# Performance work log

Hardware: AMD Instinct MI355X
Metric: run time of the kernel (lower is better)

Reference implementation:

```python
import jax, jax.numpy as jnp
import numpy as np

B, C, H, W = 16, 64, 32, 32
E, HEADS, FF, L = 64, 4, 256, 3
NO_UNIT, INB = 6, 58
LN_EPS = 1e-5


def setup_inputs() -> dict:
    key = jax.random.key(0)
    ks = jax.random.split(key, 16)
    x = jax.random.normal(ks[0], (B, C, H, W), jnp.float32)
    # channel 58 = in-bounds everywhere; channel 6 = no-unit flag (Bernoulli 0.5)
    x = x.at[:, INB].set(1.0)
    x = x.at[:, NO_UNIT].set(jax.random.bernoulli(ks[1], 0.5, (B, H, W)).astype(jnp.float32))
    s = 0.05
    return {
        'x': x,
        'embed_w': jax.random.normal(ks[2], (C + 2, E), jnp.float32) * s,
        'embed_b': jnp.zeros((E,), jnp.float32),
        'ln1_w': jnp.ones((L, E), jnp.float32),
        'ln1_b': jnp.zeros((L, E), jnp.float32),
        'in_proj_w': jax.random.normal(ks[3], (L, 3 * E, E), jnp.float32) * s,
        'in_proj_b': jnp.zeros((L, 3 * E), jnp.float32),
        'out_w': jax.random.normal(ks[4], (L, E, E), jnp.float32) * s,
        'out_b': jnp.zeros((L, E), jnp.float32),
        'ln2_w': jnp.ones((L, E), jnp.float32),
        'ln2_b': jnp.zeros((L, E), jnp.float32),
        'ff1_w': jax.random.normal(ks[5], (L, E, FF), jnp.float32) * s,
        'ff1_b': jnp.zeros((L, FF), jnp.float32),
        'ff2_w': jax.random.normal(ks[6], (L, FF, E), jnp.float32) * s,
        'ff2_b': jnp.zeros((L, E), jnp.float32),
    }


def _layer_norm(x, w, b):
    mu = jnp.mean(x, axis=-1, keepdims=True)
    var = jnp.mean(jnp.square(x - mu), axis=-1, keepdims=True)
    return (x - mu) * jax.lax.rsqrt(var + LN_EPS) * w + b


def reference(x, embed_w, embed_b, ln1_w, ln1_b, in_proj_w, in_proj_b,
              out_w, out_b, ln2_w, ln2_b, ff1_w, ff1_b, ff2_w, ff2_b):
    Bn, Cn, Hn, Wn = x.shape
    S = Hn * Wn
    # position features (H == W here, matching torch tile/t() layout)
    ly = jnp.linspace(-1.0, 1.0, Hn)
    lx = jnp.linspace(-1.0, 1.0, Wn)
    pos = jnp.stack([jnp.tile(ly, (Wn, 1)), jnp.tile(lx, (Hn, 1)).T], axis=0)  # [2,H,W]
    xf = jnp.concatenate([x, jnp.broadcast_to(pos, (Bn, 2, Hn, Wn))], axis=1)
    xs = xf.reshape(Bn, Cn + 2, S).transpose(0, 2, 1)  # [B,S,C+2]

    # empty-space mask + vectorized squash (stable sort packs kept tokens first)
    empty = (xs[..., NO_UNIT] != 0) & (xs[..., INB] != 0)  # True = empty/masked
    keep = ~empty
    order = jnp.argsort(empty.astype(jnp.int32), axis=1, stable=True)  # [B,S]
    x_sq = jnp.take_along_axis(xs, order[:, :, None], axis=1)  # [B,S,C+2]
    n_keep = jnp.sum(keep, axis=1)
    pad = jnp.arange(S)[None, :] >= n_keep[:, None]  # True = padded key
    # (torch squashes to max(n_keep); padding to S is mathematically identical
    #  since padded rows are masked as keys and discarded on unsquash)
    bias = jnp.where(pad, -1e30, 0.0)[:, None, None, :]  # [B,1,1,S]

    h = x_sq @ embed_w + embed_b  # [B,S,E]
    dh = E // HEADS
    scale = 1.0 / float(np.sqrt(dh))
    for l in range(L):
        # identity_map_reordering: pre-norm attention
        a_in = _layer_norm(h, ln1_w[l], ln1_b[l])
        qkv = a_in @ in_proj_w[l].T + in_proj_b[l]
        q, k, v = jnp.split(qkv, 3, axis=-1)
        q = q.reshape(Bn, S, HEADS, dh)
        k = k.reshape(Bn, S, HEADS, dh)
        v = v.reshape(Bn, S, HEADS, dh)
        scores = jnp.einsum('bqhd,bkhd->bhqk', q, k) * scale + bias
        attn = jax.nn.softmax(scores, axis=-1)
        o = jnp.einsum('bhqk,bkhd->bqhd', attn, v).reshape(Bn, S, E)
        h = h + (o @ out_w[l].T + out_b[l])
        # pre-norm feed-forward (exact GELU, as nn.GELU default)
        f_in = _layer_norm(h, ln2_w[l], ln2_b[l])
        ff = jax.nn.gelu(f_in @ ff1_w[l] + ff1_b[l], approximate=False) @ ff2_w[l] + ff2_b[l]
        h = h + ff

    # unsquash: inverse permutation, zero at empty positions
    inv = jnp.argsort(order, axis=1)
    out = jnp.take_along_axis(h, inv[:, :, None], axis=1) * keep[:, :, None].astype(h.dtype)
    return out.transpose(0, 2, 1).reshape(Bn, E, Hn, Wn)
```

## Files before the change

kernel.cpp:

```cpp
#include <hip/hip_runtime.h>
#include <hip/hip_bf16.h>


#define BB 16
#define SS 1024
#define NT (BB*SS)

typedef short bf8 __attribute__((ext_vector_type(8)));
typedef float f4 __attribute__((ext_vector_type(4)));
typedef unsigned short u16;
typedef unsigned short us4 __attribute__((ext_vector_type(4)));

#define MFMA(a,b,c) __builtin_amdgcn_mfma_f32_16x16x32_bf16(a,b,c,0,0,0)

__device__ __forceinline__ float b2f(u16 u){
  union { unsigned int i; float f; } v; v.i = ((unsigned int)u) << 16; return v.f;
}
__device__ __forceinline__ u16 f2b(float f){
  union { float f; unsigned int i; } v; v.f = f;
  unsigned int x = v.i;
  return (u16)((x + 0x7FFFu + ((x >> 16) & 1u)) >> 16);
}
__device__ __forceinline__ unsigned int pkbf2(float a, float b){
  __hip_bfloat162 h = __float22bfloat162_rn(make_float2(a, b));
  union { __hip_bfloat162 h; unsigned int u; } c; c.h = h; return c.u;
}
__device__ __forceinline__ int probe_f32(const void* ln1w){
  return ((const u16*)ln1w)[0] == 0;
}
__device__ __forceinline__ float ldf(const void* p, int i, int isf32){
  return isf32 ? ((const float*)p)[i] : b2f(((const u16*)p)[i]);
}
__device__ __forceinline__ bf8 ldbf8(const void* p, int idx, int isf32){
  if (!isf32) return *(const bf8*)((const u16*)p + idx);
  const float4* s = (const float4*)((const float*)p + idx);
  float4 v0 = s[0], v1 = s[1];
  bf8 r;
  r[0] = (short)f2b(v0.x); r[1] = (short)f2b(v0.y);
  r[2] = (short)f2b(v0.z); r[3] = (short)f2b(v0.w);
  r[4] = (short)f2b(v1.x); r[5] = (short)f2b(v1.y);
  r[6] = (short)f2b(v1.z); r[7] = (short)f2b(v1.w);
  return r;
}
__device__ __forceinline__ float gelu(float x){
  float y = 1.5957691216f * x * (1.f + 0.044715f * x * x);
  float e = __expf(y);
  return x - x * __builtin_amdgcn_rcpf(e + 1.f);
}

#define O_L1W  64
#define O_L1B  256
#define O_IPW  448
#define O_IPB  37312
#define O_OW   37888
#define O_OWB  50176
#define O_L2W  50368
#define O_L2B  50560
#define O_F1B  50752
#define O_F2B  51520

__device__ __forceinline__ void cv(u16* dst, const void* src, int n, int isf32,
                                   int tid, int nth){
  if (isf32){
    const float* s = (const float*)src;
    for (int i = tid; i < n; i += nth) dst[i] = f2b(s[i]);
  } else {
    const u16* s = (const u16*)src;
    for (int i = tid; i < n; i += nth) dst[i] = s[i];
  }
}

__device__ __forceinline__ void qkv_core(bf8 a0, bf8 a1, bf8 b0, bf8 b1,
    int j, float bj, int lane, int bb4, int sw,
    u16* __restrict__ qb, u16* __restrict__ kb, u16* __restrict__ vt)
{
  int quad = lane >> 4;
  f4 acc = {0.f,0.f,0.f,0.f};
  acc = MFMA(a0, b0, acc);
  acc = MFMA(a1, b1, acc);
  if (j < 128){
    u16* dst = (j < 64) ? qb : kb;
    int jj = j & 63; int hd = jj >> 4, d = jj & 15;
    int base = (bb4 + hd)*1024 + sw + quad*4;
    #pragma unroll
    for (int r = 0; r < 4; r++) dst[((base + r) << 4) + d] = f2b(acc[r] + bj);
  } else {
    int jj = j - 128; int hd = jj >> 4, d = jj & 15;
    us4 pk;
    #pragma unroll
    for (int r = 0; r < 4; r++) pk[r] = f2b(acc[r] + bj);
    *(us4*)(vt + ((bb4 + hd)*16 + d)*1024 + sw + quad*4) = pk;
  }
}

__device__ __forceinline__ void ln_to_lds(const f4* hf, int lane,
    const u16* __restrict__ w, const u16* __restrict__ bs, u16* als)
{
  int col = lane & 15, quad = lane >> 4;
  float sm[4], sq[4];
  #pragma unroll
  for (int r = 0; r < 4; r++){
    float a = 0.f, q2 = 0.f;
    #pragma unroll
    for (int f = 0; f < 4; f++){ float v = hf[f][r]; a += v; q2 += v*v; }
    sm[r] = a; sq[r] = q2;
  }
  #pragma unroll
  for (int off = 1; off < 16; off <<= 1){
    #pragma unroll
    for (int r = 0; r < 4; r++){
      sm[r] += __shfl_xor(sm[r], off, 64);
      sq[r] += __shfl_xor(sq[r], off, 64);
    }
  }
  #pragma unroll
  for (int r = 0; r < 4; r++){
    float m = sm[r] * 0.015625f;
    float rstd = rsqrtf(fmaxf(sq[r]*0.015625f - m*m, 0.f) + 1e-5f);
    sm[r] = m; sq[r] = rstd;
  }
  #pragma unroll
  for (int f = 0; f < 4; f++){
    int n = f*16 + col;
    float ww = b2f(w[n]), bb = b2f(bs[n]);
    #pragma unroll
    for (int r = 0; r < 4; r++)
      als[(quad*4 + r)*72 + n] = f2b((hf[f][r] - sm[r])*sq[r]*ww + bb);
  }
}

__device__ __forceinline__ void ln4(f4 val, int wave, int col, int quad,
    const u16* __restrict__ w, const u16* __restrict__ bs,
    u16* als, float (*lnred)[16][2])
{
  float sm[4], sq[4];
  #pragma unroll
  for (int r = 0; r < 4; r++){ sm[r] = val[r]; sq[r] = val[r]*val[r]; }
  #pragma unroll
  for (int off = 1; off < 16; off <<= 1){
    #pragma unroll
    for (int r = 0; r < 4; r++){
      sm[r] += __shfl_xor(sm[r], off, 64);
      sq[r] += __shfl_xor(sq[r], off, 64);
    }
  }
  if (col == 0){
    #pragma unroll
    for (int r = 0; r < 4; r++){
      lnred[wave][quad*4 + r][0] = sm[r];
      lnred[wave][quad*4 + r][1] = sq[r];
    }
  }
  __syncthreads();
  int n = wave*16 + col;
  float ww = b2f(w[n]), bb = b2f(bs[n]);
  #pragma unroll
  for (int r = 0; r < 4; r++){
    int row = quad*4 + r;
    float s0 = lnred[0][row][0] + lnred[1][row][0] + lnred[2][row][0] + lnred[3][row][0];
    float q0 = lnred[0][row][1] + lnred[1][row][1] + lnred[2][row][1] + lnred[3][row][1];
    float m = s0 * 0.015625f;
    float rs = rsqrtf(fmaxf(q0*0.015625f - m*m, 0.f) + 1e-5f);
    als[row*72 + n] = f2b((val[r] - m)*rs*ww + bb);
  }
}

__global__ __launch_bounds__(256) void k0(
    const void* __restrict__ x,    const void* __restrict__ ewS,
    const void* __restrict__ ebS,  const void* __restrict__ l1wS,
    const void* __restrict__ l1bS, const void* __restrict__ ipwS,
    const void* __restrict__ ipbS, const void* __restrict__ owS,
    const void* __restrict__ owbS, const void* __restrict__ l2wS,
    const void* __restrict__ l2bS, const void* __restrict__ f1wS,
    const void* __restrict__ f1bS, const void* __restrict__ f2wS,
    const void* __restrict__ f2bS,
    u16* __restrict__ cb, u16* __restrict__ f1t, u16* __restrict__ f2t,
    float* __restrict__ h, int* __restrict__ nk, u16* __restrict__ cidx,
    u16* __restrict__ qb, u16* __restrict__ kb, u16* __restrict__ vt,
    void* __restrict__ outp, int out_elems)
{
  __shared__ __align__(16) u16 xs[4][16*104];
  __shared__ __align__(16) u16 als[4][16*72];
  __shared__ __align__(16) u16 ews[64*96];
  __shared__ __align__(16) u16 wsm[384];
  __shared__ int wtot[4];
  __shared__ u16 lcidx[1024];
  int tid = threadIdx.x;
  int lane = tid & 63, wave = tid >> 6;
  int col = lane & 15, quad = lane >> 4;
  int isf32 = probe_f32(l1wS);

  if (blockIdx.x >= 256){
    int gtid = (blockIdx.x - 256)*256 + tid;
    int nth  = 768*256;
    for (int i = gtid; i < 3*256*64; i += nth){
      int l = i / (256*64); int r = i % (256*64); int n = r / 64, k = r % 64;
      f1t[i] = f2b(ldf(f1wS, (l*64 + k)*256 + n, isf32));
    }
    for (int i = gtid; i < 3*64*256; i += nth){
      int l = i / (64*256); int r = i % (64*256); int n = r / 256, k = r % 256;
      f2t[i] = f2b(ldf(f2wS, (l*256 + k)*64 + n, isf32));
    }
    cv(cb + O_L1W, l1wS, 192,   isf32, gtid, nth);
    cv(cb + O_L1B, l1bS, 192,   isf32, gtid, nth);
    cv(cb + O_IPW, ipwS, 36864, isf32, gtid, nth);
    cv(cb + O_IPB, ipbS, 576,   isf32, gtid, nth);
    cv(cb + O_OW,  owS,  12288, isf32, gtid, nth);
    cv(cb + O_OWB, owbS, 192,   isf32, gtid, nth);
    cv(cb + O_L2W, l2wS, 192,   isf32, gtid, nth);
    cv(cb + O_L2B, l2bS, 192,   isf32, gtid, nth);
    cv(cb + O_F1B, f1bS, 768,   isf32, gtid, nth);
    cv(cb + O_F2B, f2bS, 192,   isf32, gtid, nth);
    int words = isf32 ? out_elems : (out_elems >> 1);
    unsigned int* op = (unsigned int*)outp;
    for (int i = gtid; i < words; i += nth) op[i] = 0u;
    return;
  }

  int b = blockIdx.x >> 4;
  int seg = blockIdx.x & 15;

  int kpl[4]; int c = 0;
  #pragma unroll
  for (int j = 0; j < 4; j++){
    int s4 = tid*4 + j;
    float x6  = ldf(x, ((b << 6) + 6)*1024 + s4, isf32);
    float x58 = ldf(x, ((b << 6) + 58)*1024 + s4, isf32);
    int k = (x6 != 0.f && x58 != 0.f) ? 0 : 1;
    kpl[j] = k; c += k;
  }
  #pragma unroll
  for (int j = 0; j < 4; j++) lcidx[tid*4 + j] = 0;
  int incl = c;
  #pragma unroll
  for (int off = 1; off < 64; off <<= 1){
    int v = __shfl_up(incl, off, 64);
    if (lane >= off) incl += v;
  }
  if (lane == 63) wtot[wave] = incl;
  __syncthreads();
  int prefix = 0;
  #pragma unroll
  for (int w2 = 0; w2 < 4; w2++) if (w2 < wave) prefix += wtot[w2];
  int excl = prefix + incl - c;
  int total = wtot[0] + wtot[1] + wtot[2] + wtot[3];
  {
    int p = excl;
    #pragma unroll
    for (int j = 0; j < 4; j++)
      if (kpl[j]){ lcidx[p] = (u16)(tid*4 + j); p++; }
  }
  __syncthreads();
  if (seg == 0){
    #pragma unroll
    for (int j = 0; j < 4; j++){
      int idx = tid*4 + j;
      cidx[(b << 10) + idx] = lcidx[idx];
    }
    if (tid == 0) nk[b] = total;
  }
  int base = seg * 64;
  if (base >= total) return;

  for (int i = tid; i < 64*96; i += 256){
    int n = i / 96, cc = i - n*96;
    ews[i] = (cc < 66) ? f2b(ldf(ewS, cc*64 + n, isf32)) : (u16)0;
  }
  for (int i = tid; i < 384; i += 256){
    float v;
    if (i < 64)       v = ldf(ebS,  i,       isf32);
    else if (i < 128) v = ldf(l1wS, i - 64,  isf32);
    else if (i < 192) v = ldf(l1bS, i - 128, isf32);
    else              v = ldf(ipbS, i - 192, isf32);
    wsm[i] = f2b(v);
  }
  __syncthreads();

  int slot0 = base + wave*16;
  int slotc = slot0 + col;
  int s = lcidx[slotc];
  u16* axs = xs[wave];
  #pragma unroll
  for (int i = 0; i < 16; i++){
    int cch = quad*16 + i;
    axs[col*104 + cch] = f2b(ldf(x, ((b << 6) + cch)*1024 + s, isf32));
  }
  #pragma unroll
  for (int i = 0; i < 8; i++){
    int cch = 64 + quad*8 + i;
    float v = 0.f;
    if (cch == 64)      v = -1.f + (2.f/31.f)*(float)(s & 31);
    else if (cch == 65) v = -1.f + (2.f/31.f)*(float)((s >> 5) & 31);
    axs[col*104 + cch] = f2b(v);
  }
  bf8 af[3];
  #pragma unroll
  for (int kc = 0; kc < 3; kc++) af[kc] = *(const bf8*)(axs + col*104 + kc*32 + quad*8);
  f4 hf[4];
  #pragma unroll
  for (int f = 0; f < 4; f++){
    f4 acc = {0.f,0.f,0.f,0.f};
    #pragma unroll
    for (int kc = 0; kc < 3; kc++){
      bf8 bfr = *(const bf8*)(ews + (f*16+col)*96 + kc*32 + quad*8);
      acc = MFMA(af[kc], bfr, acc);
    }
    float bias = b2f(wsm[f*16 + col]);
    #pragma unroll
    for (int r = 0; r < 4; r++){
      acc[r] += bias;
      h[((b << 10) + slot0 + quad*4 + r)*64 + f*16 + col] = acc[r];
    }
    hf[f] = acc;
  }
  ln_to_lds(hf, lane, wsm + 64, wsm + 128, als[wave]);
  bf8 a0 = *(const bf8*)(als[wave] + col*72 + quad*8);
  bf8 a1 = *(const bf8*)(als[wave] + col*72 + 32 + quad*8);
  #pragma unroll
  for (int jt = 0; jt < 12; jt++){
    int j = jt*16 + col;
    bf8 b0 = ldbf8(ipwS, (jt*16+col)*64 + quad*8, isf32);
    bf8 b1 = ldbf8(ipwS, (jt*16+col)*64 + 32 + quad*8, isf32);
    qkv_core(a0, a1, b0, b1, j, b2f(wsm[192 + j]), lane, b << 2, slot0, qb, kb, vt);
  }
}

__global__ __launch_bounds__(256) void k_layer(
    float* __restrict__ h, const u16* __restrict__ cb, int l, int nl,
    const u16* __restrict__ f1l, const u16* __restrict__ f2l,
    const u16* __restrict__ qbR, const u16* __restrict__ kbR,
    const u16* __restrict__ vtR,
    u16* __restrict__ qbW, u16* __restrict__ kbW, u16* __restrict__ vtW,
    const int* __restrict__ nk, const u16* __restrict__ cidx,
    void* __restrict__ outp, const void* __restrict__ dtype_probe, int last)
{
  __shared__ __align__(16) u16 smem[6528];
  __shared__ float lnred[4][16][2];
  u16* plds = smem;
  u16* gls  = smem;
  u16* ols  = smem + 4224;
  u16* als  = smem + 5376;

  int tid = threadIdx.x;
  int lane = tid & 63, wave = tid >> 6;
  int col = lane & 15, quad = lane >> 4;
  int b = blockIdx.x >> 6;
  int tb = (blockIdx.x & 63) * 16;
  int total = nk[b];
  if (tb >= total) return;
  int nfull = total & ~31;
  int tw = (b << 10) + tb;

  {
    int bh = (b << 2) + wave;
    const u16* qbase = qbR + (bh << 14);
    const u16* kbase = kbR + (bh << 14);
    const u16* vbase = vtR + (bh << 14);
    bf8 qf = {0,0,0,0,0,0,0,0};
    if (quad < 2) qf = *(const bf8*)(qbase + ((tb + col) << 4) + quad*8);
    f4 oacc = {0.f,0.f,0.f,0.f};
    float l4v[4] = {0.f,0.f,0.f,0.f};
    u16* pw = plds + wave*640;
    int kc = 0;
    for (; kc < nfull; kc += 32){
      bf8 vf = *(const bf8*)(vbase + col*1024 + kc + quad*8);
      #pragma unroll
      for (int t = 0; t < 2; t++){
        bf8 kf = {0,0,0,0,0,0,0,0};
        if (quad < 2) kf = *(const bf8*)(kbase + ((kc + t*16 + col) << 4) + quad*8);
        f4 sc = {0.f,0.f,0.f,0.f};
        sc = MFMA(qf, kf, sc);
        float p0 = __expf(fminf(sc[0]*0.25f, 60.f));
        float p1 = __expf(fminf(sc[1]*0.25f, 60.f));
        float p2 = __expf(fminf(sc[2]*0.25f, 60.f));
        float p3 = __expf(fminf(sc[3]*0.25f, 60.f));
        l4v[0] += p0; l4v[1] += p1; l4v[2] += p2; l4v[3] += p3;
        unsigned int u01 = pkbf2(p0, p1), u23 = pkbf2(p2, p3);
        int off = t*16 + col;
        pw[(quad*4 + 0)*40 + off] = (u16)u01;
        pw[(quad*4 + 1)*40 + off] = (u16)(u01 >> 16);
        pw[(quad*4 + 2)*40 + off] = (u16)u23;
        pw[(quad*4 + 3)*40 + off] = (u16)(u23 >> 16);
      }
      bf8 pf = *(const bf8*)(pw + col*40 + quad*8);
      oacc = MFMA(pf, vf, oacc);
    }
    if (kc < total){
      bf8 vf = *(const bf8*)(vbase + col*1024 + kc + quad*8);
      #pragma unroll
      for (int t = 0; t < 2; t++){
        bf8 kf = {0,0,0,0,0,0,0,0};
        int key = kc + t*16 + col;
        if (quad < 2) kf = *(const bf8*)(kbase + (key << 4) + quad*8);
        f4 sc = {0.f,0.f,0.f,0.f};
        sc = MFMA(qf, kf, sc);
        float kpv = (key < total) ? 1.f : 0.f;
        float p0 = kpv * __expf(fminf(sc[0]*0.25f, 60.f));
        float p1 = kpv * __expf(fminf(sc[1]*0.25f, 60.f));
        float p2 = kpv * __expf(fminf(sc[2]*0.25f, 60.f));
        float p3 = kpv * __expf(fminf(sc[3]*0.25f, 60.f));
        l4v[0] += p0; l4v[1] += p1; l4v[2] += p2; l4v[3] += p3;
        unsigned int u01 = pkbf2(p0, p1), u23 = pkbf2(p2, p3);
        int off = t*16 + col;
        pw[(quad*4 + 0)*40 + off] = (u16)u01;
        pw[(quad*4 + 1)*40 + off] = (u16)(u01 >> 16);
        pw[(quad*4 + 2)*40 + off] = (u16)u23;
        pw[(quad*4 + 3)*40 + off] = (u16)(u23 >> 16);
      }
      bf8 pf = *(const bf8*)(pw + col*40 + quad*8);
      oacc = MFMA(pf, vf, oacc);
    }
    #pragma unroll
    for (int off = 1; off < 16; off <<= 1)
      #pragma unroll
      for (int r = 0; r < 4; r++) l4v[r] += __shfl_xor(l4v[r], off, 64);
    #pragma unroll
    for (int r = 0; r < 4; r++){
      float rd = __builtin_amdgcn_rcpf(fmaxf(l4v[r], 1e-30f));
      ols[(quad*4 + r)*72 + wave*16 + col] = f2b(oacc[r] * rd);
    }
  }
  __syncthreads();

  {
    const u16* ow     = cb + O_OW  + l*4096;
    const u16* obias  = cb + O_OWB + l*64;
    const u16* f1b    = cb + O_F1B + l*256;
    const u16* f2bias = cb + O_F2B + l*64;
    int f = wave;
    bf8 af0 = *(const bf8*)(ols + col*72 + quad*8);
    bf8 af1 = *(const bf8*)(ols + col*72 + 32 + quad*8);
    f4 acc = {0.f,0.f,0.f,0.f};
    acc = MFMA(af0, *(const bf8*)(ow + (f*16+col)*64 + quad*8), acc);
    acc = MFMA(af1, *(const bf8*)(ow + (f*16+col)*64 + 32 + quad*8), acc);
    float bo = b2f(obias[f*16 + col]);
    f4 hfA;
    #pragma unroll
    for (int r = 0; r < 4; r++)
      hfA[r] = h[(tw + quad*4 + r)*64 + f*16 + col] + acc[r] + bo;
    ln4(hfA, wave, col, quad, cb + O_L2W + l*64, cb + O_L2B + l*64, als, lnred);
    __syncthreads();
    bf8 a0 = *(const bf8*)(als + col*72 + quad*8);
    bf8 a1 = *(const bf8*)(als + col*72 + 32 + quad*8);
    #pragma unroll
    for (int j = 0; j < 4; j++){
      int ft = wave*4 + j;
      f4 fa = {0.f,0.f,0.f,0.f};
      fa = MFMA(a0, *(const bf8*)(f1l + (ft*16+col)*64 + quad*8), fa);
      fa = MFMA(a1, *(const bf8*)(f1l + (ft*16+col)*64 + 32 + quad*8), fa);
      int n = ft*16 + col;
      float bb = b2f(f1b[n]);
      float g0 = gelu(fa[0] + bb), g1 = gelu(fa[1] + bb);
      float g2 = gelu(fa[2] + bb), g3 = gelu(fa[3] + bb);
      unsigned int u01 = pkbf2(g0, g1), u23 = pkbf2(g2, g3);
      gls[(quad*4 + 0)*264 + n] = (u16)u01;
      gls[(quad*4 + 1)*264 + n] = (u16)(u01 >> 16);
      gls[(quad*4 + 2)*264 + n] = (u16)u23;
      gls[(quad*4 + 3)*264 + n] = (u16)(u23 >> 16);
    }
    __syncthreads();
    bf8 gfr[8];
    #pragma unroll
    for (int kc = 0; kc < 8; kc++)
      gfr[kc] = *(const bf8*)(gls + col*264 + kc*32 + quad*8);
    f4 acc2 = {0.f,0.f,0.f,0.f};
    #pragma unroll
    for (int kc = 0; kc < 8; kc++)
      acc2 = MFMA(gfr[kc], *(const bf8*)(f2l + (f*16+col)*256 + kc*32 + quad*8), acc2);
    float b2v = b2f(f2bias[f*16 + col]);
    f4 hv;
    #pragma unroll
    for (int r = 0; r < 4; r++)
      hv[r] = hfA[r] + acc2[r] + b2v;
    if (last){
      int isf32 = probe_f32(dtype_probe);
      #pragma unroll
      for (int r = 0; r < 4; r++){
        int slot = tb + quad*4 + r;
        if (slot < total){
          int s = cidx[(b << 10) + slot];
          long idx = (long)((b << 6) + f*16 + col)*1024 + s;
          if (isf32) ((float*)outp)[idx] = hv[r];
          else       ((u16*)outp)[idx]   = f2b(hv[r]);
        }
      }
    } else {
      #pragma unroll
      for (int r = 0; r < 4; r++)
        h[(tw + quad*4 + r)*64 + f*16 + col] = hv[r];
      ln4(hv, wave, col, quad, cb + O_L1W + nl*64, cb + O_L1B + nl*64, als, lnred);
      __syncthreads();
      const u16* ipw = cb + O_IPW + nl*12288;
      const u16* ipb = cb + O_IPB + nl*192;
      bf8 qa0 = *(const bf8*)(als + col*72 + quad*8);
      bf8 qa1 = *(const bf8*)(als + col*72 + 32 + quad*8);
      #pragma unroll
      for (int j = 0; j < 3; j++){
        int jt = wave*3 + j;
        int jj = jt*16 + col;
        bf8 b0 = *(const bf8*)(ipw + (jt*16+col)*64 + quad*8);
        bf8 b1 = *(const bf8*)(ipw + (jt*16+col)*64 + 32 + quad*8);
        qkv_core(qa0, qa1, b0, b1, jj, b2f(ipb[jj]), lane, b << 2, tb,
                 qbW, kbW, vtW);
      }
    }
  }
}

extern "C" void kernel_launch(void* const* d_in, const int* in_sizes, int n_in,
                              void* d_out, int out_size, void* d_ws, size_t ws_size,
                              hipStream_t stream)
{
  (void)in_sizes; (void)n_in; (void)ws_size;
  char* ws = (char*)d_ws;
  float* h     = (float*)(ws + 0);
  int*   nk    = (int*)(ws + 4194304);
  u16*   cidx  = (u16*)(ws + 4194368);
  u16*   qA    = (u16*)(ws + 4292672);
  u16*   kA    = (u16*)(ws + 6389824);
  u16*   vA    = (u16*)(ws + 8486976);
  u16*   qB    = (u16*)(ws + 10584128);
  u16*   kB    = (u16*)(ws + 12681280);
  u16*   vB    = (u16*)(ws + 14778432);
  u16*   f1t   = (u16*)(ws + 16875584);
  u16*   f2t   = (u16*)(ws + 16973888);
  u16*   cb    = (u16*)(ws + 17072192);

  k0<<<1024, 256, 0, stream>>>(d_in[0], d_in[1], d_in[2], d_in[3], d_in[4],
                               d_in[5], d_in[6], d_in[7], d_in[8], d_in[9],
                               d_in[10], d_in[11], d_in[12], d_in[13], d_in[14],
                               cb, f1t, f2t, h, nk, cidx,
                               qA, kA, vA, d_out, out_size);
  for (int l = 0; l < 3; l++){
    int nl = (l < 2) ? (l + 1) : 0;
    u16 *qR, *kR, *vR, *qW, *kW, *vW;
    if ((l & 1) == 0){ qR = qA; kR = kA; vR = vA; qW = qB; kW = kB; vW = vB; }
    else             { qR = qB; kR = kB; vR = vB; qW = qA; kW = kA; vW = vA; }
    k_layer<<<NT/16, 256, 0, stream>>>(h, cb, l, nl,
                                       f1t + l*16384, f2t + l*16384,
                                       qR, kR, vR, qW, kW, vW,
                                       nk, cidx, d_out, d_in[3],
                                       (l == 2) ? 1 : 0);
  }
}
```

Before: 200.3 us.

## Fuse embed and all layers into one cooperative persistent kernel with grid sync

Replaces the four separate launches (embed/QKV kernel plus three per-layer kernels) with a single cooperative kernel. It uses grid-wide syncs between layers and has each block loop over several 16-token tiles. Weight conversion and output zeroing move to extra blocks beyond the first 256, overlapping with the embedding work. The aim is to remove launch gaps and kernel-boundary drains. In exchange, the grid is capped at what stays resident, which reduces parallelism per layer, and a grid sync costs time. If the cooperative launch fails, the old multi-kernel path runs.

Result: no change. 199.0 us (-0.7%).

```diff
diff --git a/kernel.cpp b/kernel.cpp
--- a/kernel.cpp
+++ b/kernel.cpp
@@ -1,6 +1,9 @@
 #include <hip/hip_runtime.h>
 #include <hip/hip_bf16.h>
-
+#include <hip/hip_cooperative_groups.h>
+
+
+namespace cg = cooperative_groups;
 
 #define BB 16
 #define SS 1024
@@ -58,6 +61,16 @@
 #define O_L2B  50560
 #define O_F1B  50752
 #define O_F2B  51520
+
+#define SH_WORDS 14216
+#define A_XS    0
+#define A_EWS   6656
+#define A_WSM   12800
+#define A_LCIDX 13184
+#define A_WTOT  14208
+#define L_OLS   4224
+#define L_ALS   5376
+#define L_LNRED 6528
 
 __device__ __forceinline__ void cv(u16* dst, const void* src, int n, int isf32,
                                    int tid, int nth){
@@ -165,7 +178,352 @@
   }
 }
 
-__global__ __launch_bounds__(256) void k0(
+__global__ __launch_bounds__(256, 2) void kall(
+    const void* __restrict__ x,    const void* __restrict__ ewS,
+    const void* __restrict__ ebS,  const void* __restrict__ l1wS,
+    const void* __restrict__ l1bS, const void* __restrict__ ipwS,
+    const void* __restrict__ ipbS, const void* __restrict__ owS,
+    const void* __restrict__ owbS, const void* __restrict__ l2wS,
+    const void* __restrict__ l2bS, const void* __restrict__ f1wS,
+    const void* __restrict__ f1bS, const void* __restrict__ f2wS,
+    const void* __restrict__ f2bS,
+    u16* __restrict__ cb, u16* __restrict__ f1t, u16* __restrict__ f2t,
+    float* __restrict__ h, int* __restrict__ nk, u16* __restrict__ cidx,
+    u16* __restrict__ qA, u16* __restrict__ kA, u16* __restrict__ vA,
+    u16* __restrict__ qB, u16* __restrict__ kB, u16* __restrict__ vB,
+    void* __restrict__ outp, int out_elems)
+{
+  __shared__ __align__(16) u16 SH[SH_WORDS];
+  int tid = threadIdx.x;
+  int lane = tid & 63, wave = tid >> 6;
+  int col = lane & 15, quad = lane >> 4;
+  int isf32 = probe_f32(l1wS);
+
+  if (blockIdx.x >= 256){
+    int nconv = (int)gridDim.x - 256;
+    int gtid = ((int)blockIdx.x - 256)*256 + tid;
+    int nth  = nconv*256;
+    for (int i = gtid; i < 3*256*64; i += nth){
+      int l = i / (256*64); int r = i % (256*64); int n = r / 64, k = r % 64;
+      f1t[i] = f2b(ldf(f1wS, (l*64 + k)*256 + n, isf32));
+    }
+    for (int i = gtid; i < 3*64*256; i += nth){
+      int l = i / (64*256); int r = i % (64*256); int n = r / 256, k = r % 256;
+      f2t[i] = f2b(ldf(f2wS, (l*256 + k)*64 + n, isf32));
+    }
+    cv(cb + O_L1W, l1wS, 192,   isf32, gtid, nth);
+    cv(cb + O_L1B, l1bS, 192,   isf32, gtid, nth);
+    cv(cb + O_IPW, ipwS, 36864, isf32, gtid, nth);
+    cv(cb + O_IPB, ipbS, 576,   isf32, gtid, nth);
+    cv(cb + O_OW,  owS,  12288, isf32, gtid, nth);
+    cv(cb + O_OWB, owbS, 192,   isf32, gtid, nth);
+    cv(cb + O_L2W, l2wS, 192,   isf32, gtid, nth);
+    cv(cb + O_L2B, l2bS, 192,   isf32, gtid, nth);
+    cv(cb + O_F1B, f1bS, 768,   isf32, gtid, nth);
+    cv(cb + O_F2B, f2bS, 192,   isf32, gtid, nth);
+    int words = isf32 ? out_elems : (out_elems >> 1);
+    unsigned int* op = (unsigned int*)outp;
+    for (int i = gtid; i < words; i += nth) op[i] = 0u;
+  } else {
+    u16* lcidx = SH + A_LCIDX;
+    int* wtot  = (int*)(SH + A_WTOT);
+    int b = blockIdx.x >> 4;
+    int seg = blockIdx.x & 15;
+
+    int kpl[4]; int c = 0;
+    #pragma unroll
+    for (int j = 0; j < 4; j++){
+      int s4 = tid*4 + j;
+      float x6  = ldf(x, ((b << 6) + 6)*1024 + s4, isf32);
+      float x58 = ldf(x, ((b << 6) + 58)*1024 + s4, isf32);
+      int k = (x6 != 0.f && x58 != 0.f) ? 0 : 1;
+      kpl[j] = k; c += k;
+    }
+    #pragma unroll
+    for (int j = 0; j < 4; j++) lcidx[tid*4 + j] = 0;
+    int incl = c;
+    #pragma unroll
+    for (int off = 1; off < 64; off <<= 1){
+      int v = __shfl_up(incl, off, 64);
+      if (lane >= off) incl += v;
+    }
+    if (lane == 63) wtot[wave] = incl;
+    __syncthreads();
+    int prefix = 0;
+    #pragma unroll
+    for (int w2 = 0; w2 < 4; w2++) if (w2 < wave) prefix += wtot[w2];
+    int excl = prefix + incl - c;
+    int total = wtot[0] + wtot[1] + wtot[2] + wtot[3];
+    {
+      int p = excl;
+      #pragma unroll
+      for (int j = 0; j < 4; j++)
+        if (kpl[j]){ lcidx[p] = (u16)(tid*4 + j); p++; }
+    }
+    __syncthreads();
+    if (seg == 0){
+      #pragma unroll
+      for (int j = 0; j < 4; j++){
+        int idx = tid*4 + j;
+        cidx[(b << 10) + idx] = lcidx[idx];
+      }
+      if (tid == 0) nk[b] = total;
+    }
+    int base = seg * 64;
+    if (base < total){
+      u16* ews = SH + A_EWS;
+      u16* wsm = SH + A_WSM;
+      for (int i = tid; i < 64*96; i += 256){
+        int n = i / 96, cc = i - n*96;
+        ews[i] = (cc < 66) ? f2b(ldf(ewS, cc*64 + n, isf32)) : (u16)0;
+      }
+      for (int i = tid; i < 384; i += 256){
+        float v;
+        if (i < 64)       v = ldf(ebS,  i,       isf32);
+        else if (i < 128) v = ldf(l1wS, i - 64,  isf32);
+        else if (i < 192) v = ldf(l1bS, i - 128, isf32);
+        else              v = ldf(ipbS, i - 192, isf32);
+        wsm[i] = f2b(v);
+      }
+      __syncthreads();
+
+      int slot0 = base + wave*16;
+      int slotc = slot0 + col;
+      int s = lcidx[slotc];
+      u16* axs = SH + A_XS + wave*1664;
+      #pragma unroll
+      for (int i = 0; i < 16; i++){
+        int cch = quad*16 + i;
+        axs[col*104 + cch] = f2b(ldf(x, ((b << 6) + cch)*1024 + s, isf32));
+      }
+      #pragma unroll
+      for (int i = 0; i < 8; i++){
+        int cch = 64 + quad*8 + i;
+        float v = 0.f;
+        if (cch == 64)      v = -1.f + (2.f/31.f)*(float)(s & 31);
+        else if (cch == 65) v = -1.f + (2.f/31.f)*(float)((s >> 5) & 31);
+        axs[col*104 + cch] = f2b(v);
+      }
+      bf8 af[3];
+      #pragma unroll
+      for (int kc = 0; kc < 3; kc++) af[kc] = *(const bf8*)(axs + col*104 + kc*32 + quad*8);
+      f4 hf[4];
+      #pragma unroll
+      for (int f = 0; f < 4; f++){
+        f4 acc = {0.f,0.f,0.f,0.f};
+        #pragma unroll
+        for (int kc = 0; kc < 3; kc++){
+          bf8 bfr = *(const bf8*)(ews + (f*16+col)*96 + kc*32 + quad*8);
+          acc = MFMA(af[kc], bfr, acc);
+        }
+        float bias = b2f(wsm[f*16 + col]);
+        #pragma unroll
+        for (int r = 0; r < 4; r++){
+          acc[r] += bias;
+          h[((b << 10) + slot0 + quad*4 + r)*64 + f*16 + col] = acc[r];
+        }
+        hf[f] = acc;
+      }
+      u16* alsA = axs;
+      ln_to_lds(hf, lane, wsm + 64, wsm + 128, alsA);
+      bf8 a0 = *(const bf8*)(alsA + col*72 + quad*8);
+      bf8 a1 = *(const bf8*)(alsA + col*72 + 32 + quad*8);
+      #pragma unroll
+      for (int jt = 0; jt < 12; jt++){
+        int j = jt*16 + col;
+        bf8 b0 = ldbf8(ipwS, (jt*16+col)*64 + quad*8, isf32);
+        bf8 b1 = ldbf8(ipwS, (jt*16+col)*64 + 32 + quad*8, isf32);
+        qkv_core(a0, a1, b0, b1, j, b2f(wsm[192 + j]), lane, b << 2, slot0,
+                 qA, kA, vA);
+      }
+    }
+  }
+
+  int tpb = 1024 / (int)gridDim.x;
+  for (int l = 0; l < 3; l++){
+    cg::this_grid().sync();
+    int nl = (l < 2) ? (l + 1) : 0;
+    int last = (l == 2);
+    const u16* f1l = f1t + l*16384;
+    const u16* f2l = f2t + l*16384;
+    const u16 *qbR, *kbR, *vtR; u16 *qbW, *kbW, *vtW;
+    if ((l & 1) == 0){ qbR = qA; kbR = kA; vtR = vA; qbW = qB; kbW = kB; vtW = vB; }
+    else             { qbR = qB; kbR = kB; vtR = vB; qbW = qA; kbW = kA; vtW = vA; }
+
+    for (int h2 = 0; h2 < tpb; h2++){
+      int tileid = (int)blockIdx.x * tpb + h2;
+      int b = tileid >> 6;
+      int tb = (tileid & 63) * 16;
+      int total = nk[b];
+      if (tb >= total) continue;
+      __syncthreads();
+
+      u16* plds = SH;
+      u16* gls  = SH;
+      u16* ols  = SH + L_OLS;
+      u16* alsL = SH + L_ALS;
+      float (*lnred)[16][2] = (float(*)[16][2])(SH + L_LNRED);
+      int nfull = total & ~31;
+      int tw = (b << 10) + tb;
+
+      {
+        int bh = (b << 2) + wave;
+        const u16* qbase = qbR + (bh << 14);
+        const u16* kbase = kbR + (bh << 14);
+        const u16* vbase = vtR + (bh << 14);
+        bf8 qf = {0,0,0,0,0,0,0,0};
+        if (quad < 2) qf = *(const bf8*)(qbase + ((tb + col) << 4) + quad*8);
+        f4 oacc = {0.f,0.f,0.f,0.f};
+        float l4v[4] = {0.f,0.f,0.f,0.f};
+        u16* pw = plds + wave*640;
+        int kc = 0;
+        for (; kc < nfull; kc += 32){
+          bf8 vf = *(const bf8*)(vbase + col*1024 + kc + quad*8);
+          #pragma unroll
+          for (int t = 0; t < 2; t++){
+            bf8 kf = {0,0,0,0,0,0,0,0};
+            if (quad < 2) kf = *(const bf8*)(kbase + ((kc + t*16 + col) << 4) + quad*8);
+            f4 sc = {0.f,0.f,0.f,0.f};
+            sc = MFMA(qf, kf, sc);
+            float p0 = __expf(fminf(sc[0]*0.25f, 60.f));
+            float p1 = __expf(fminf(sc[1]*0.25f, 60.f));
+            float p2 = __expf(fminf(sc[2]*0.25f, 60.f));
+            float p3 = __expf(fminf(sc[3]*0.25f, 60.f));
+            l4v[0] += p0; l4v[1] += p1; l4v[2] += p2; l4v[3] += p3;
+            unsigned int u01 = pkbf2(p0, p1), u23 = pkbf2(p2, p3);
+            int off = t*16 + col;
+            pw[(quad*4 + 0)*40 + off] = (u16)u01;
+            pw[(quad*4 + 1)*40 + off] = (u16)(u01 >> 16);
+            pw[(quad*4 + 2)*40 + off] = (u16)u23;
+            pw[(quad*4 + 3)*40 + off] = (u16)(u23 >> 16);
+          }
+          bf8 pf = *(const bf8*)(pw + col*40 + quad*8);
+          oacc = MFMA(pf, vf, oacc);
+        }
+        if (kc < total){
+          bf8 vf = *(const bf8*)(vbase + col*1024 + kc + quad*8);
+          #pragma unroll
+          for (int t = 0; t < 2; t++){
+            bf8 kf = {0,0,0,0,0,0,0,0};
+            int key = kc + t*16 + col;
+            if (quad < 2) kf = *(const bf8*)(kbase + (key << 4) + quad*8);
+            f4 sc = {0.f,0.f,0.f,0.f};
+            sc = MFMA(qf, kf, sc);
+            float kpv = (key < total) ? 1.f : 0.f;
+            float p0 = kpv * __expf(fminf(sc[0]*0.25f, 60.f));
+            float p1 = kpv * __expf(fminf(sc[1]*0.25f, 60.f));
+            float p2 = kpv * __expf(fminf(sc[2]*0.25f, 60.f));
+            float p3 = kpv * __expf(fminf(sc[3]*0.25f, 60.f));
+            l4v[0] += p0; l4v[1] += p1; l4v[2] += p2; l4v[3] += p3;
+            unsigned int u01 = pkbf2(p0, p1), u23 = pkbf2(p2, p3);
+            int off = t*16 + col;
+            pw[(quad*4 + 0)*40 + off] = (u16)u01;
+            pw[(quad*4 + 1)*40 + off] = (u16)(u01 >> 16);
+            pw[(quad*4 + 2)*40 + off] = (u16)u23;
+            pw[(quad*4 + 3)*40 + off] = (u16)(u23 >> 16);
+          }
+          bf8 pf = *(const bf8*)(pw + col*40 + quad*8);
+          oacc = MFMA(pf, vf, oacc);
+        }
+        #pragma unroll
+        for (int off = 1; off < 16; off <<= 1)
+          #pragma unroll
+          for (int r = 0; r < 4; r++) l4v[r] += __shfl_xor(l4v[r], off, 64);
+        #pragma unroll
+        for (int r = 0; r < 4; r++){
+          float rd = __builtin_amdgcn_rcpf(fmaxf(l4v[r], 1e-30f));
+          ols[(quad*4 + r)*72 + wave*16 + col] = f2b(oacc[r] * rd);
+        }
+      }
+      __syncthreads();
+
+      {
+        const u16* ow     = cb + O_OW  + l*4096;
+        const u16* obias  = cb + O_OWB + l*64;
+        const u16* f1b    = cb + O_F1B + l*256;
+        const u16* f2bias = cb + O_F2B + l*64;
+        int f = wave;
+        bf8 af0 = *(const bf8*)(ols + col*72 + quad*8);
+        bf8 af1 = *(const bf8*)(ols + col*72 + 32 + quad*8);
+        f4 acc = {0.f,0.f,0.f,0.f};
+        acc = MFMA(af0, *(const bf8*)(ow + (f*16+col)*64 + quad*8), acc);
+        acc = MFMA(af1, *(const bf8*)(ow + (f*16+col)*64 + 32 + quad*8), acc);
+        float bo = b2f(obias[f*16 + col]);
+        f4 hfA;
+        #pragma unroll
+        for (int r = 0; r < 4; r++)
+          hfA[r] = h[(tw + quad*4 + r)*64 + f*16 + col] + acc[r] + bo;
+        ln4(hfA, wave, col, quad, cb + O_L2W + l*64, cb + O_L2B + l*64, alsL, lnred);
+        __syncthreads();
+        bf8 a0 = *(const bf8*)(alsL + col*72 + quad*8);
+        bf8 a1 = *(const bf8*)(alsL + col*72 + 32 + quad*8);
+        #pragma unroll
+        for (int j = 0; j < 4; j++){
+          int ft = wave*4 + j;
+          f4 fa = {0.f,0.f,0.f,0.f};
+          fa = MFMA(a0, *(const bf8*)(f1l + (ft*16+col)*64 + quad*8), fa);
+          fa = MFMA(a1, *(const bf8*)(f1l + (ft*16+col)*64 + 32 + quad*8), fa);
+          int n = ft*16 + col;
+          float bb = b2f(f1b[n]);
+          float g0 = gelu(fa[0] + bb), g1 = gelu(fa[1] + bb);
+          float g2 = gelu(fa[2] + bb), g3 = gelu(fa[3] + bb);
+          unsigned int u01 = pkbf2(g0, g1), u23 = pkbf2(g2, g3);
+          gls[(quad*4 + 0)*264 + n] = (u16)u01;
+          gls[(quad*4 + 1)*264 + n] = (u16)(u01 >> 16);
+          gls[(quad*4 + 2)*264 + n] = (u16)u23;
+          gls[(quad*4 + 3)*264 + n] = (u16)(u23 >> 16);
+        }
+        __syncthreads();
+        bf8 gfr[8];
+        #pragma unroll
+        for (int kc = 0; kc < 8; kc++)
+          gfr[kc] = *(const bf8*)(gls + col*264 + kc*32 + quad*8);
+        f4 acc2 = {0.f,0.f,0.f,0.f};
+        #pragma unroll
+        for (int kc = 0; kc < 8; kc++)
+          acc2 = MFMA(gfr[kc], *(const bf8*)(f2l + (f*16+col)*256 + kc*32 + quad*8), acc2);
+        float b2v = b2f(f2bias[f*16 + col]);
+        f4 hv;
+        #pragma unroll
+        for (int r = 0; r < 4; r++)
+          hv[r] = hfA[r] + acc2[r] + b2v;
+        if (last){
+          #pragma unroll
+          for (int r = 0; r < 4; r++){
+            int slot = tb + quad*4 + r;
+            if (slot < total){
+              int s = cidx[(b << 10) + slot];
+              long idx = (long)((b << 6) + f*16 + col)*1024 + s;
+              if (isf32) ((float*)outp)[idx] = hv[r];
+              else       ((u16*)outp)[idx]   = f2b(hv[r]);
+            }
+          }
+        } else {
+          #pragma unroll
+          for (int r = 0; r < 4; r++)
+            h[(tw + quad*4 + r)*64 + f*16 + col] = hv[r];
+          ln4(hv, wave, col, quad, cb + O_L1W + nl*64, cb + O_L1B + nl*64, alsL, lnred);
+          __syncthreads();
+          const u16* ipw = cb + O_IPW + nl*12288;
+          const u16* ipb = cb + O_IPB + nl*192;
+          bf8 qa0 = *(const bf8*)(alsL + col*72 + quad*8);
+          bf8 qa1 = *(const bf8*)(alsL + col*72 + 32 + quad*8);
+          #pragma unroll
+          for (int j = 0; j < 3; j++){
+            int jt = wave*3 + j;
+            int jj = jt*16 + col;
+            bf8 b0 = *(const bf8*)(ipw + (jt*16+col)*64 + quad*8);
+            bf8 b1 = *(const bf8*)(ipw + (jt*16+col)*64 + 32 + quad*8);
+            qkv_core(qa0, qa1, b0, b1, jj, b2f(ipb[jj]), lane, b << 2, tb,
+                     qbW, kbW, vtW);
+          }
+        }
+      }
+    }
+  }
+}
+
+__global__ __launch_bounds__(256) void k0f(
     const void* __restrict__ x,    const void* __restrict__ ewS,
     const void* __restrict__ ebS,  const void* __restrict__ l1wS,
     const void* __restrict__ l1bS, const void* __restrict__ ipwS,
@@ -325,7 +683,7 @@
   }
 }
 
-__global__ __launch_bounds__(256) void k_layer(
+__global__ __launch_bounds__(256) void k_layerf(
     float* __restrict__ h, const u16* __restrict__ cb, int l, int nl,
     const u16* __restrict__ f1l, const u16* __restrict__ f2l,
     const u16* __restrict__ qbR, const u16* __restrict__ kbR,
@@ -526,20 +884,54 @@
   u16*   f2t   = (u16*)(ws + 16973888);
   u16*   cb    = (u16*)(ws + 17072192);
 
-  k0<<<1024, 256, 0, stream>>>(d_in[0], d_in[1], d_in[2], d_in[3], d_in[4],
-                               d_in[5], d_in[6], d_in[7], d_in[8], d_in[9],
-                               d_in[10], d_in[11], d_in[12], d_in[13], d_in[14],
-                               cb, f1t, f2t, h, nk, cidx,
-                               qA, kA, vA, d_out, out_size);
-  for (int l = 0; l < 3; l++){
-    int nl = (l < 2) ? (l + 1) : 0;
-    u16 *qR, *kR, *vR, *qW, *kW, *vW;
-    if ((l & 1) == 0){ qR = qA; kR = kA; vR = vA; qW = qB; kW = kB; vW = vB; }
-    else             { qR = qB; kR = kB; vR = vB; qW = qA; kW = kA; vW = vA; }
-    k_layer<<<NT/16, 256, 0, stream>>>(h, cb, l, nl,
-                                       f1t + l*16384, f2t + l*16384,
-                                       qR, kR, vR, qW, kW, vW,
-                                       nk, cidx, d_out, d_in[3],
-                                       (l == 2) ? 1 : 0);
-  }
-}
+  int occ = 0;
+  hipError_t qe = hipOccupancyMaxActiveBlocksPerMultiprocessor(&occ, kall, 256, 0);
+  int grid = 0;
+  if (qe == hipSuccess){
+    if (occ >= 4)      grid = 1024;
+    else if (occ >= 2) grid = 512;
+  }
+
+  bool done = false;
+  if (grid){
+    const void* a0  = d_in[0];  const void* a1  = d_in[1];
+    const void* a2  = d_in[2];  const void* a3  = d_in[3];
+    const void* a4  = d_in[4];  const void* a5  = d_in[5];
+    const void* a6  = d_in[6];  const void* a7  = d_in[7];
+    const void* a8  = d_in[8];  const void* a9  = d_in[9];
+    const void* a10 = d_in[10]; const void* a11 = d_in[11];
+    const void* a12 = d_in[12]; const void* a13 = d_in[13];
+    const void* a14 = d_in[14];
+    void* op = d_out;
+    int   oe = out_size;
+    void* args[] = {
+      &a0, &a1, &a2, &a3, &a4, &a5, &a6, &a7, &a8, &a9, &a10, &a11, &a12,
+      &a13, &a14,
+      &cb, &f1t, &f2t, &h, &nk, &cidx,
+      &qA, &kA, &vA, &qB, &kB, &vB,
+      &op, &oe
+    };
+    hipError_t le = hipLaunchCooperativeKernel(kall, dim3(grid), dim3(256),
+                                               args, 0, stream);
+    done = (le == hipSuccess);
+  }
+
+  if (!done){
+    k0f<<<1024, 256, 0, stream>>>(d_in[0], d_in[1], d_in[2], d_in[3], d_in[4],
+                                  d_in[5], d_in[6], d_in[7], d_in[8], d_in[9],
+                                  d_in[10], d_in[11], d_in[12], d_in[13], d_in[14],
+                                  cb, f1t, f2t, h, nk, cidx,
+                                  qA, kA, vA, d_out, out_size);
+    for (int l = 0; l < 3; l++){
+      int nl = (l < 2) ? (l + 1) : 0;
+      u16 *qR, *kR, *vR, *qW, *kW, *vW;
+      if ((l & 1) == 0){ qR = qA; kR = kA; vR = vA; qW = qB; kW = kB; vW = vB; }
+      else             { qR = qB; kR = kB; vR = vB; qW = qA; kW = kA; vW = vA; }
+      k_layerf<<<NT/16, 256, 0, stream>>>(h, cb, l, nl,
+                                          f1t + l*16384, f2t + l*16384,
+                                          qR, kR, vR, qW, kW, vW,
+                                          nk, cidx, d_out, d_in[3],
+                                          (l == 2) ? 1 : 0);
+    }
+  }
+}
```
